# Performance work log

Hardware: AMD Instinct MI355X
Metric: run time of the kernel (lower is better)

## Reference

```python
import jax, jax.numpy as jnp
import numpy as np

B, T, D = 2, 2048, 1024
E, H, K = 8, 2048, 2  # n_experts, expert_dim, n_active_experts


def setup_inputs() -> dict:
    key = jax.random.key(0)
    ks = jax.random.split(key, 5)
    s = 0.02
    return {
        "x": jax.random.normal(ks[0], (B, T, D), dtype=jnp.float32),
        "gate_w": jax.random.normal(ks[1], (E, D), dtype=jnp.float32) * s,
        "w1": jax.random.normal(ks[2], (E, H, D), dtype=jnp.float32) * s,
        "w2": jax.random.normal(ks[3], (E, D, H), dtype=jnp.float32) * s,
        "w3": jax.random.normal(ks[4], (E, H, D), dtype=jnp.float32) * s,
    }


def reference(x, gate_w, w1, w2, w3):
    Bb, Tt, Dd = x.shape
    xf = x.reshape(-1, Dd)                       # [N, D]
    logits = xf @ gate_w.T                       # [N, E]
    probs = jax.nn.softmax(logits, axis=-1)
    vals, idx = jax.lax.top_k(probs, K)          # [N, K]
    w = vals / (vals.sum(-1, keepdims=True) + 1e-8)
    onehot = jax.nn.one_hot(idx, E, dtype=xf.dtype)  # [N, K, E]
    comb = jnp.einsum('nk,nke->ne', w, onehot)   # per-token per-expert combine weight
    # Dense expert eval (same math as masked loop): SwiGLU per expert
    h = jnp.einsum('nd,ehd->neh', xf, w1)        # [N, E, H]
    g = jnp.einsum('nd,ehd->neh', xf, w3)
    eo = jnp.einsum('neh,edh->ned', jax.nn.silu(h) * g, w2)  # [N, E, D]
    out = jnp.einsum('ned,ne->nd', eo, comb)
    return out.reshape(Bb, Tt, Dd)
```

## Files before the change

kernel.cpp:

```cpp
#include <hip/hip_runtime.h>
#include <stdint.h>

#define N_TOK 4096
#define DIM   1024
#define NEXP  8
#define HDIM  2048
#define NSLOT 8192
#define PADSLOT 10240
#define MAXT1 40
#define MAXT2 80

typedef __attribute__((ext_vector_type(8))) short  short8;
typedef __attribute__((ext_vector_type(4))) float  f32x4;

__device__ inline unsigned short f2bf(float f) {
  union { float f; uint32_t u; } v; v.f = f;
  uint32_t u = v.u;
  u += 0x7fffu + ((u >> 16) & 1u);
  return (unsigned short)(u >> 16);
}

__device__ inline void gload_lds16(const void* g, void* l) {
  __builtin_amdgcn_global_load_lds(
      (const __attribute__((address_space(1))) uint32_t*)g,
      (__attribute__((address_space(3))) uint32_t*)l, 16, 0, 0);
}

__global__ __launch_bounds__(256) void cvt_all_kernel(const float* __restrict__ x,
                                                      const float* __restrict__ w1,
                                                      const float* __restrict__ w2,
                                                      const float* __restrict__ w3,
                                                      unsigned short* __restrict__ xb,
                                                      unsigned short* __restrict__ w1b,
                                                      unsigned short* __restrict__ w2b,
                                                      unsigned short* __restrict__ w3b) {
  const int NX = N_TOK * DIM / 4;
  const int NW = NEXP * HDIM * DIM / 4;
  int i = blockIdx.x * blockDim.x + threadIdx.x;
  int stride = gridDim.x * blockDim.x;
  int total = NX + 3 * NW;
  for (; i < total; i += stride) {
    const float* s; unsigned short* d; int j;
    if (i < NX)               { s = x;  d = xb;  j = i; }
    else if (i < NX + NW)     { s = w1; d = w1b; j = i - NX; }
    else if (i < NX + 2 * NW) { s = w2; d = w2b; j = i - NX - NW; }
    else                      { s = w3; d = w3b; j = i - NX - 2 * NW; }
    float4 f = reinterpret_cast<const float4*>(s)[j];
    ushort4 o;
    o.x = f2bf(f.x); o.y = f2bf(f.y); o.z = f2bf(f.z); o.w = f2bf(f.w);
    reinterpret_cast<ushort4*>(d)[j] = o;
  }
}

__global__ __launch_bounds__(256) void gate_kernel(const float* __restrict__ x,
                                                   const float* __restrict__ gw,
                                                   int* __restrict__ tok_e,
                                                   float* __restrict__ tok_w) {
  __shared__ float gws[NEXP * DIM];
  int tid = threadIdx.x;
  for (int i = tid; i < NEXP * DIM; i += 256) gws[i] = gw[i];
  __syncthreads();
  int lane = tid & 63;
  int token = blockIdx.x * 4 + (tid >> 6);
  const float* xr = x + (size_t)token * DIM;
  float acc[NEXP];
#pragma unroll
  for (int e = 0; e < NEXP; ++e) acc[e] = 0.f;
  for (int i = 0; i < DIM / 64; ++i) {
    float xv = xr[i * 64 + lane];
#pragma unroll
    for (int e = 0; e < NEXP; ++e) acc[e] += xv * gws[e * DIM + i * 64 + lane];
  }
#pragma unroll
  for (int off = 32; off > 0; off >>= 1) {
#pragma unroll
    for (int e = 0; e < NEXP; ++e) acc[e] += __shfl_xor(acc[e], off);
  }
  if (lane == 0) {
    float m = acc[0];
#pragma unroll
    for (int e = 1; e < NEXP; ++e) m = fmaxf(m, acc[e]);
    float ex[NEXP], Z = 0.f;
#pragma unroll
    for (int e = 0; e < NEXP; ++e) { ex[e] = expf(acc[e] - m); Z += ex[e]; }
    int b0 = 0; float v0 = ex[0];
#pragma unroll
    for (int e = 1; e < NEXP; ++e) if (ex[e] > v0) { v0 = ex[e]; b0 = e; }
    int b1 = -1; float v1 = -1.f;
#pragma unroll
    for (int e = 0; e < NEXP; ++e) if (e != b0 && ex[e] > v1) { v1 = ex[e]; b1 = e; }
    float p0 = v0 / Z, p1 = v1 / Z;
    float s = p0 + p1 + 1e-8f;
    tok_e[token * 2 + 0] = b0; tok_e[token * 2 + 1] = b1;
    tok_w[token * 2 + 0] = p0 / s; tok_w[token * 2 + 1] = p1 / s;
  }
}

__global__ __launch_bounds__(1024) void route_kernel(const int* __restrict__ tok_e,
                                                     const float* __restrict__ tok_w,
                                                     int* __restrict__ slot_tok,
                                                     float* __restrict__ slot_w,
                                                     int* __restrict__ tile1_e,
                                                     int* __restrict__ tile1_rb,
                                                     int* __restrict__ tile2_e,
                                                     int* __restrict__ tile2_rb,
                                                     int* __restrict__ ntile_g) {
  __shared__ int cnt[NEXP], cur[NEXP];
  __shared__ int total_sh;
  int tid = threadIdx.x;
  if (tid < NEXP) cnt[tid] = 0;
  __syncthreads();
  for (int n = tid; n < N_TOK; n += 1024) {
    atomicAdd(&cnt[tok_e[2 * n]], 1);
    atomicAdd(&cnt[tok_e[2 * n + 1]], 1);
  }
  __syncthreads();
  if (tid == 0) {
    int o = 0, n1 = 0, n2 = 0;
    for (int e = 0; e < NEXP; ++e) {
      cur[e] = o;
      int padded = (cnt[e] + 255) & ~255;
      for (int rb = o; rb < o + padded; rb += 256) { tile1_e[n1] = e; tile1_rb[n1] = rb; ++n1; }
      for (int rb = o; rb < o + padded; rb += 128) { tile2_e[n2] = e; tile2_rb[n2] = rb; ++n2; }
      o += padded;
    }
    ntile_g[0] = n1; ntile_g[1] = n2;
    total_sh = o;
  }
  __syncthreads();
  int total = total_sh;
  for (int s = tid; s < total; s += 1024) { slot_tok[s] = 0; slot_w[s] = 0.f; }
  __syncthreads();
  for (int n = tid; n < N_TOK; n += 1024) {
#pragma unroll
    for (int k = 0; k < 2; ++k) {
      int e = tok_e[2 * n + k];
      int p = atomicAdd(&cur[e], 1);
      slot_tok[p] = n;
      slot_w[p] = tok_w[2 * n + k];
    }
  }
}

__global__ __launch_bounds__(512, 2) void gemm1_kernel(const unsigned short* __restrict__ xb,
                                                       const unsigned short* __restrict__ w1b,
                                                       const unsigned short* __restrict__ w3b,
                                                       const int* __restrict__ slot_tok,
                                                       const int* __restrict__ tile1_e,
                                                       const int* __restrict__ tile1_rb,
                                                       const int* __restrict__ ntile_g,
                                                       unsigned short* __restrict__ hidden) {
  int tile = blockIdx.x >> 4;
  int ct   = blockIdx.x & 15;
  if (tile >= ntile_g[0]) return;
  int e = tile1_e[tile];
  int rowBase = tile1_rb[tile];

  __shared__ alignas(16) unsigned short As[2][256 * 64];
  __shared__ alignas(16) unsigned short B1s[2][128 * 64];
  __shared__ alignas(16) unsigned short B3s[2][128 * 64];
  __shared__ int toks[256];

  int tid = threadIdx.x;
  if (tid < 256) toks[tid] = slot_tok[rowBase + tid];
  __syncthreads();

  int wave = tid >> 6, lane = tid & 63;
  int wr = (wave >> 1) * 64;
  int wc = (wave & 1) * 64;
  int sub = lane >> 3;
  int swcol = (((lane & 7) ^ sub) << 3);

  const size_t wbase = (size_t)e * HDIM * DIM;
  const unsigned short* aptr[4];
  const unsigned short* b1ptr[2];
  const unsigned short* b3ptr[2];
#pragma unroll
  for (int i = 0; i < 4; ++i) {
    int r = (wave + i * 8) * 8 + sub;
    aptr[i] = xb + (size_t)toks[r] * DIM + swcol;
  }
#pragma unroll
  for (int i = 0; i < 2; ++i) {
    int r = (wave + i * 8) * 8 + sub;
    b1ptr[i] = w1b + wbase + (size_t)(ct * 128 + r) * DIM + swcol;
    b3ptr[i] = w3b + wbase + (size_t)(ct * 128 + r) * DIM + swcol;
  }

  f32x4 hacc[4][4], gacc[4][4];
#pragma unroll
  for (int m = 0; m < 4; ++m)
#pragma unroll
    for (int n = 0; n < 4; ++n) {
      hacc[m][n] = (f32x4){0.f, 0.f, 0.f, 0.f};
      gacc[m][n] = (f32x4){0.f, 0.f, 0.f, 0.f};
    }

  gload_lds16(aptr[0], &As[0][(wave + 0) * 512]);
  gload_lds16(aptr[1], &As[0][(wave + 8) * 512]);
  gload_lds16(aptr[2], &As[0][(wave + 16) * 512]);
  gload_lds16(aptr[3], &As[0][(wave + 24) * 512]);
  gload_lds16(b1ptr[0], &B1s[0][wave * 512]);
  gload_lds16(b1ptr[1], &B1s[0][(wave + 8) * 512]);
  gload_lds16(b3ptr[0], &B3s[0][wave * 512]);
  gload_lds16(b3ptr[1], &B3s[0][(wave + 8) * 512]);

  const int NKT = DIM / 64;
  int key = (lane & 7) << 3;
  int l15 = lane & 15;
  int pc0 = ((lane >> 4) * 8) ^ key;
  int pc1 = (32 + (lane >> 4) * 8) ^ key;

  for (int kt = 0; kt < NKT; ++kt) {
    int c = kt & 1;
    int nk = (kt + 1) * 64;
    bool pre = (kt + 1 < NKT);

    __builtin_amdgcn_sched_barrier(0);
    __builtin_amdgcn_s_barrier();
    __builtin_amdgcn_sched_barrier(0);
    if (pre) {
      gload_lds16(aptr[0] + nk, &As[c ^ 1][(wave + 0) * 512]);
      gload_lds16(aptr[1] + nk, &As[c ^ 1][(wave + 8) * 512]);
      asm volatile("s_waitcnt vmcnt(4)" ::: "memory");
    } else {
      asm volatile("s_waitcnt vmcnt(2)" ::: "memory");
    }
    __builtin_amdgcn_sched_barrier(0);
    __builtin_amdgcn_s_barrier();
    __builtin_amdgcn_sched_barrier(0);

    short8 a0[4], a1[4], bv[4];
#pragma unroll
    for (int m = 0; m < 4; ++m)
      a0[m] = *(const short8*)&As[c][(wr + m * 16 + l15) * 64 + pc0];
#pragma unroll
    for (int n = 0; n < 4; ++n)
      bv[n] = *(const short8*)&B1s[c][(wc + n * 16 + l15) * 64 + pc0];
    if (pre) {
      gload_lds16(aptr[2] + nk, &As[c ^ 1][(wave + 16) * 512]);
      gload_lds16(aptr[3] + nk, &As[c ^ 1][(wave + 24) * 512]);
    }
    __builtin_amdgcn_s_setprio(1);
#pragma unroll
    for (int m = 0; m < 4; ++m)
#pragma unroll
      for (int n = 0; n < 4; ++n)
        hacc[m][n] = __builtin_amdgcn_mfma_f32_16x16x32_bf16(a0[m], bv[n], hacc[m][n], 0, 0, 0);
    __builtin_amdgcn_s_setprio(0);

#pragma unroll
    for (int m = 0; m < 4; ++m)
      a1[m] = *(const short8*)&As[c][(wr + m * 16 + l15) * 64 + pc1];
#pragma unroll
    for (int n = 0; n < 4; ++n)
      bv[n] = *(const short8*)&B1s[c][(wc + n * 16 + l15) * 64 + pc1];
    if (pre) {
      gload_lds16(b1ptr[0] + nk, &B1s[c ^ 1][wave * 512]);
      gload_lds16(b1ptr[1] + nk, &B1s[c ^ 1][(wave + 8) * 512]);
    }
    __builtin_amdgcn_s_setprio(1);
#pragma unroll
    for (int m = 0; m < 4; ++m)
#pragma unroll
      for (int n = 0; n < 4; ++n)
        hacc[m][n] = __builtin_amdgcn_mfma_f32_16x16x32_bf16(a1[m], bv[n], hacc[m][n], 0, 0, 0);
    __builtin_amdgcn_s_setprio(0);

    if (pre) asm volatile("s_waitcnt vmcnt(6)" ::: "memory");
    else     asm volatile("s_waitcnt vmcnt(0)" ::: "memory");
    __builtin_amdgcn_sched_barrier(0);
    __builtin_amdgcn_s_barrier();
    __builtin_amdgcn_sched_barrier(0);

#pragma unroll
    for (int n = 0; n < 4; ++n)
      bv[n] = *(const short8*)&B3s[c][(wc + n * 16 + l15) * 64 + pc0];
    if (pre) {
      gload_lds16(b3ptr[0] + nk, &B3s[c ^ 1][wave * 512]);
      gload_lds16(b3ptr[1] + nk, &B3s[c ^ 1][(wave + 8) * 512]);
    }
    __builtin_amdgcn_s_setprio(1);
#pragma unroll
    for (int m = 0; m < 4; ++m)
#pragma unroll
      for (int n = 0; n < 4; ++n)
        gacc[m][n] = __builtin_amdgcn_mfma_f32_16x16x32_bf16(a0[m], bv[n], gacc[m][n], 0, 0, 0);
    __builtin_amdgcn_s_setprio(0);

#pragma unroll
    for (int n = 0; n < 4; ++n)
      bv[n] = *(const short8*)&B3s[c][(wc + n * 16 + l15) * 64 + pc1];
    __builtin_amdgcn_s_setprio(1);
#pragma unroll
    for (int m = 0; m < 4; ++m)
#pragma unroll
      for (int n = 0; n < 4; ++n)
        gacc[m][n] = __builtin_amdgcn_mfma_f32_16x16x32_bf16(a1[m], bv[n], gacc[m][n], 0, 0, 0);
    __builtin_amdgcn_s_setprio(0);
  }

  int cbase = ct * 128 + wc;
#pragma unroll
  for (int m = 0; m < 4; ++m) {
#pragma unroll
    for (int q = 0; q < 4; ++q) {
      int r = wr + m * 16 + ((lane >> 4) * 4 + q);
      size_t rowoff = (size_t)(rowBase + r) * HDIM + cbase;
#pragma unroll
      for (int n = 0; n < 4; ++n) {
        float h = hacc[m][n][q], g = gacc[m][n][q];
        float val = (h / (1.f + expf(-h))) * g;
        hidden[rowoff + n * 16 + (lane & 15)] = f2bf(val);
      }
    }
  }
}

__global__ __launch_bounds__(256, 2) void gemm2_kernel(const unsigned short* __restrict__ hidden,
                                                       const unsigned short* __restrict__ w2b,
                                                       const int* __restrict__ slot_tok,
                                                       const float* __restrict__ slot_w,
                                                       const int* __restrict__ tile2_e,
                                                       const int* __restrict__ tile2_rb,
                                                       const int* __restrict__ ntile_g,
                                                       float* __restrict__ out) {
  int tile = blockIdx.x >> 3;
  int ct   = blockIdx.x & 7;
  if (tile >= ntile_g[1]) return;
  int e = tile2_e[tile];
  int rowBase = tile2_rb[tile];

  __shared__ alignas(16) unsigned short As[2][128 * 64];
  __shared__ alignas(16) unsigned short Bs[2][128 * 64];
  __shared__ int   toks[128];
  __shared__ float wgt[128];

  int tid = threadIdx.x;
  if (tid < 128) {
    toks[tid] = slot_tok[rowBase + tid];
    wgt[tid]  = slot_w[rowBase + tid];
  }
  __syncthreads();

  int wave = tid >> 6, lane = tid & 63;
  int wr = (wave >> 1) * 64, wc = (wave & 1) * 64;
  int sub = lane >> 3;
  int swcol = (((lane & 7) ^ sub) << 3);

  const size_t w2base = (size_t)e * DIM * HDIM;
  const unsigned short* aptr[4];
  const unsigned short* bptr[4];
#pragma unroll
  for (int i = 0; i < 4; ++i) {
    int r = (wave + i * 4) * 8 + sub;
    aptr[i] = hidden + (size_t)(rowBase + r) * HDIM + swcol;
    bptr[i] = w2b + w2base + (size_t)(ct * 128 + r) * HDIM + swcol;
  }

  f32x4 acc[4][4];
#pragma unroll
  for (int m = 0; m < 4; ++m)
#pragma unroll
    for (int n = 0; n < 4; ++n) acc[m][n] = (f32x4){0.f, 0.f, 0.f, 0.f};

#pragma unroll
  for (int i = 0; i < 4; ++i)
    gload_lds16(aptr[i], &As[0][(wave + i * 4) * 512]);
#pragma unroll
  for (int i = 0; i < 4; ++i)
    gload_lds16(bptr[i], &Bs[0][(wave + i * 4) * 512]);

  const int NKT = HDIM / 64;
  int key = (lane & 7) << 3;
  int l15 = lane & 15;
  int pc0 = ((lane >> 4) * 8) ^ key;
  int pc1 = (32 + (lane >> 4) * 8) ^ key;

  for (int kt = 0; kt < NKT; ++kt) {
    int c = kt & 1;
    int nk = (kt + 1) * 64;
    bool pre = (kt + 1 < NKT);

    __builtin_amdgcn_sched_barrier(0);
    __builtin_amdgcn_s_barrier();
    __builtin_amdgcn_sched_barrier(0);
    if (pre) {
#pragma unroll
      for (int i = 0; i < 4; ++i)
        gload_lds16(aptr[i] + nk, &As[c ^ 1][(wave + i * 4) * 512]);
      asm volatile("s_waitcnt vmcnt(4)" ::: "memory");
    } else {
      asm volatile("s_waitcnt vmcnt(0)" ::: "memory");
    }
    __builtin_amdgcn_sched_barrier(0);
    __builtin_amdgcn_s_barrier();
    __builtin_amdgcn_sched_barrier(0);

    short8 a[4], b[4];
#pragma unroll
    for (int m = 0; m < 4; ++m)
      a[m] = *(const short8*)&As[c][(wr + m * 16 + l15) * 64 + pc0];
#pragma unroll
    for (int n = 0; n < 4; ++n)
      b[n] = *(const short8*)&Bs[c][(wc + n * 16 + l15) * 64 + pc0];
    if (pre) {
#pragma unroll
      for (int i = 0; i < 4; ++i)
        gload_lds16(bptr[i] + nk, &Bs[c ^ 1][(wave + i * 4) * 512]);
    }
    __builtin_amdgcn_s_setprio(1);
#pragma unroll
    for (int m = 0; m < 4; ++m)
#pragma unroll
      for (int n = 0; n < 4; ++n)
        acc[m][n] = __builtin_amdgcn_mfma_f32_16x16x32_bf16(a[m], b[n], acc[m][n], 0, 0, 0);
    __builtin_amdgcn_s_setprio(0);

#pragma unroll
    for (int m = 0; m < 4; ++m)
      a[m] = *(const short8*)&As[c][(wr + m * 16 + l15) * 64 + pc1];
#pragma unroll
    for (int n = 0; n < 4; ++n)
      b[n] = *(const short8*)&Bs[c][(wc + n * 16 + l15) * 64 + pc1];
    __builtin_amdgcn_s_setprio(1);
#pragma unroll
    for (int m = 0; m < 4; ++m)
#pragma unroll
      for (int n = 0; n < 4; ++n)
        acc[m][n] = __builtin_amdgcn_mfma_f32_16x16x32_bf16(a[m], b[n], acc[m][n], 0, 0, 0);
    __builtin_amdgcn_s_setprio(0);
  }

  int cbase = ct * 128 + wc;
#pragma unroll
  for (int m = 0; m < 4; ++m) {
#pragma unroll
    for (int q = 0; q < 4; ++q) {
      int r = wr + m * 16 + ((lane >> 4) * 4 + q);
      float w = wgt[r];
      float* orow = out + (size_t)toks[r] * DIM + cbase;
#pragma unroll
      for (int n = 0; n < 4; ++n)
        unsafeAtomicAdd(&orow[n * 16 + (lane & 15)], acc[m][n][q] * w);
    }
  }
}

extern "C" void kernel_launch(void* const* d_in, const int* in_sizes, int n_in,
                              void* d_out, int out_size, void* d_ws, size_t ws_size,
                              hipStream_t stream) {
  const float* x  = (const float*)d_in[0];
  const float* gw = (const float*)d_in[1];
  const float* w1 = (const float*)d_in[2];
  const float* w2 = (const float*)d_in[3];
  const float* w3 = (const float*)d_in[4];
  float* out = (float*)d_out;

  uint8_t* ws = (uint8_t*)d_ws;
  size_t off = 0;
  auto alloc = [&](size_t bytes) -> void* {
    void* p = ws + off; off += (bytes + 255) & ~255ull; return p;
  };
  unsigned short* xb     = (unsigned short*)alloc((size_t)N_TOK * DIM * 2);
  unsigned short* w1b    = (unsigned short*)alloc((size_t)NEXP * HDIM * DIM * 2);
  unsigned short* w3b    = (unsigned short*)alloc((size_t)NEXP * HDIM * DIM * 2);
  unsigned short* w2b    = (unsigned short*)alloc((size_t)NEXP * DIM * HDIM * 2);
  unsigned short* hidden = (unsigned short*)alloc((size_t)PADSLOT * HDIM * 2);
  int*   tok_e    = (int*)alloc(N_TOK * 2 * 4);
  float* tok_w    = (float*)alloc(N_TOK * 2 * 4);
  int*   slot_tok = (int*)alloc(PADSLOT * 4);
  float* slot_w   = (float*)alloc(PADSLOT * 4);
  int*   tile1_e  = (int*)alloc(MAXT1 * 4);
  int*   tile1_rb = (int*)alloc(MAXT1 * 4);
  int*   tile2_e  = (int*)alloc(MAXT2 * 4);
  int*   tile2_rb = (int*)alloc(MAXT2 * 4);
  int*   ntile_g  = (int*)alloc(2 * 4);

  hipMemsetAsync(d_out, 0, (size_t)out_size * sizeof(float), stream);

  cvt_all_kernel<<<2048, 256, 0, stream>>>(x, w1, w2, w3, xb, w1b, w2b, w3b);

  gate_kernel<<<N_TOK / 4, 256, 0, stream>>>(x, gw, tok_e, tok_w);
  route_kernel<<<1, 1024, 0, stream>>>(tok_e, tok_w, slot_tok, slot_w,
                                       tile1_e, tile1_rb, tile2_e, tile2_rb, ntile_g);
  gemm1_kernel<<<MAXT1 * 16, 512, 0, stream>>>(
      xb, w1b, w3b, slot_tok, tile1_e, tile1_rb, ntile_g, hidden);
  gemm2_kernel<<<MAXT2 * 8, 256, 0, stream>>>(
      hidden, w2b, slot_tok, slot_w, tile2_e, tile2_rb, ntile_g, out);
}
```

Measured before the change: 520.5 us.

## Switch expert GEMMs to 4-stage K=32 pipeline and 8-wave gemm2 tiles

```diff
diff --git a/kernel.cpp b/kernel.cpp
--- a/kernel.cpp
+++ b/kernel.cpp
@@ -142,7 +142,7 @@
   }
 }
 
-__global__ __launch_bounds__(512, 2) void gemm1_kernel(const unsigned short* __restrict__ xb,
+__global__ __launch_bounds__(512, 1) void gemm1_kernel(const unsigned short* __restrict__ xb,
                                                        const unsigned short* __restrict__ w1b,
                                                        const unsigned short* __restrict__ w3b,
                                                        const int* __restrict__ slot_tok,
@@ -156,9 +156,9 @@
   int e = tile1_e[tile];
   int rowBase = tile1_rb[tile];
 
-  __shared__ alignas(16) unsigned short As[2][256 * 64];
-  __shared__ alignas(16) unsigned short B1s[2][128 * 64];
-  __shared__ alignas(16) unsigned short B3s[2][128 * 64];
+  __shared__ alignas(16) unsigned short As[4][256 * 32];
+  __shared__ alignas(16) unsigned short B1s[4][128 * 32];
+  __shared__ alignas(16) unsigned short B3s[4][128 * 32];
   __shared__ int toks[256];
 
   int tid = threadIdx.x;
@@ -168,23 +168,23 @@
   int wave = tid >> 6, lane = tid & 63;
   int wr = (wave >> 1) * 64;
   int wc = (wave & 1) * 64;
-  int sub = lane >> 3;
-  int swcol = (((lane & 7) ^ sub) << 3);
+  int r4  = lane >> 2;
+  int cph = lane & 3;
 
   const size_t wbase = (size_t)e * HDIM * DIM;
-  const unsigned short* aptr[4];
-  const unsigned short* b1ptr[2];
-  const unsigned short* b3ptr[2];
-#pragma unroll
-  for (int i = 0; i < 4; ++i) {
-    int r = (wave + i * 8) * 8 + sub;
-    aptr[i] = xb + (size_t)toks[r] * DIM + swcol;
-  }
+  const unsigned short* aptr[2];
+  const unsigned short* b1p;
+  const unsigned short* b3p;
 #pragma unroll
   for (int i = 0; i < 2; ++i) {
-    int r = (wave + i * 8) * 8 + sub;
-    b1ptr[i] = w1b + wbase + (size_t)(ct * 128 + r) * DIM + swcol;
-    b3ptr[i] = w3b + wbase + (size_t)(ct * 128 + r) * DIM + swcol;
+    int r = i * 128 + wave * 16 + r4;
+    aptr[i] = xb + (size_t)toks[r] * DIM + ((cph ^ (r & 3)) << 3);
+  }
+  {
+    int r = wave * 16 + r4;
+    int col = (cph ^ (r & 3)) << 3;
+    b1p = w1b + wbase + (size_t)(ct * 128 + r) * DIM + col;
+    b3p = w3b + wbase + (size_t)(ct * 128 + r) * DIM + col;
   }
 
   f32x4 hacc[4][4], gacc[4][4];
@@ -196,107 +196,58 @@
       gacc[m][n] = (f32x4){0.f, 0.f, 0.f, 0.f};
     }
 
-  gload_lds16(aptr[0], &As[0][(wave + 0) * 512]);
-  gload_lds16(aptr[1], &As[0][(wave + 8) * 512]);
-  gload_lds16(aptr[2], &As[0][(wave + 16) * 512]);
-  gload_lds16(aptr[3], &As[0][(wave + 24) * 512]);
-  gload_lds16(b1ptr[0], &B1s[0][wave * 512]);
-  gload_lds16(b1ptr[1], &B1s[0][(wave + 8) * 512]);
-  gload_lds16(b3ptr[0], &B3s[0][wave * 512]);
-  gload_lds16(b3ptr[1], &B3s[0][(wave + 8) * 512]);
-
-  const int NKT = DIM / 64;
-  int key = (lane & 7) << 3;
+  auto stage = [&](int buf, int kt) {
+    int k0 = kt * 32;
+    gload_lds16(aptr[0] + k0, &As[buf][wave * 512]);
+    gload_lds16(aptr[1] + k0, &As[buf][4096 + wave * 512]);
+    gload_lds16(b1p + k0, &B1s[buf][wave * 512]);
+    gload_lds16(b3p + k0, &B3s[buf][wave * 512]);
+  };
+
+  stage(0, 0); stage(1, 1); stage(2, 2);
+
+  const int NKT = DIM / 32;
   int l15 = lane & 15;
-  int pc0 = ((lane >> 4) * 8) ^ key;
-  int pc1 = (32 + (lane >> 4) * 8) ^ key;
+  int pcoff = (((lane >> 4) ^ (l15 & 3)) << 3);
 
   for (int kt = 0; kt < NKT; ++kt) {
-    int c = kt & 1;
-    int nk = (kt + 1) * 64;
-    bool pre = (kt + 1 < NKT);
+    int c = kt & 3;
+    int rem = NKT - 1 - kt;
 
     __builtin_amdgcn_sched_barrier(0);
     __builtin_amdgcn_s_barrier();
     __builtin_amdgcn_sched_barrier(0);
-    if (pre) {
-      gload_lds16(aptr[0] + nk, &As[c ^ 1][(wave + 0) * 512]);
-      gload_lds16(aptr[1] + nk, &As[c ^ 1][(wave + 8) * 512]);
+    if (rem >= 3) {
+      stage((kt + 3) & 3, kt + 3);
+      asm volatile("s_waitcnt vmcnt(12)" ::: "memory");
+    } else if (rem == 2) {
+      asm volatile("s_waitcnt vmcnt(8)" ::: "memory");
+    } else if (rem == 1) {
       asm volatile("s_waitcnt vmcnt(4)" ::: "memory");
     } else {
-      asm volatile("s_waitcnt vmcnt(2)" ::: "memory");
+      asm volatile("s_waitcnt vmcnt(0)" ::: "memory");
     }
     __builtin_amdgcn_sched_barrier(0);
     __builtin_amdgcn_s_barrier();
     __builtin_amdgcn_sched_barrier(0);
 
-    short8 a0[4], a1[4], bv[4];
+    short8 a[4], b1v[4], b3v[4];
 #pragma unroll
     for (int m = 0; m < 4; ++m)
-      a0[m] = *(const short8*)&As[c][(wr + m * 16 + l15) * 64 + pc0];
-#pragma unroll
-    for (int n = 0; n < 4; ++n)
-      bv[n] = *(const short8*)&B1s[c][(wc + n * 16 + l15) * 64 + pc0];
-    if (pre) {
-      gload_lds16(aptr[2] + nk, &As[c ^ 1][(wave + 16) * 512]);
-      gload_lds16(aptr[3] + nk, &As[c ^ 1][(wave + 24) * 512]);
+      a[m] = *(const short8*)&As[c][(wr + m * 16 + l15) * 32 + pcoff];
+#pragma unroll
+    for (int n = 0; n < 4; ++n) {
+      b1v[n] = *(const short8*)&B1s[c][(wc + n * 16 + l15) * 32 + pcoff];
+      b3v[n] = *(const short8*)&B3s[c][(wc + n * 16 + l15) * 32 + pcoff];
     }
     __builtin_amdgcn_s_setprio(1);
 #pragma unroll
     for (int m = 0; m < 4; ++m)
 #pragma unroll
-      for (int n = 0; n < 4; ++n)
-        hacc[m][n] = __builtin_amdgcn_mfma_f32_16x16x32_bf16(a0[m], bv[n], hacc[m][n], 0, 0, 0);
-    __builtin_amdgcn_s_setprio(0);
-
-#pragma unroll
-    for (int m = 0; m < 4; ++m)
-      a1[m] = *(const short8*)&As[c][(wr + m * 16 + l15) * 64 + pc1];
-#pragma unroll
-    for (int n = 0; n < 4; ++n)
-      bv[n] = *(const short8*)&B1s[c][(wc + n * 16 + l15) * 64 + pc1];
-    if (pre) {
-      gload_lds16(b1ptr[0] + nk, &B1s[c ^ 1][wave * 512]);
-      gload_lds16(b1ptr[1] + nk, &B1s[c ^ 1][(wave + 8) * 512]);
-    }
-    __builtin_amdgcn_s_setprio(1);
-#pragma unroll
-    for (int m = 0; m < 4; ++m)
-#pragma unroll
-      for (int n = 0; n < 4; ++n)
-        hacc[m][n] = __builtin_amdgcn_mfma_f32_16x16x32_bf16(a1[m], bv[n], hacc[m][n], 0, 0, 0);
-    __builtin_amdgcn_s_setprio(0);
-
-    if (pre) asm volatile("s_waitcnt vmcnt(6)" ::: "memory");
-    else     asm volatile("s_waitcnt vmcnt(0)" ::: "memory");
-    __builtin_amdgcn_sched_barrier(0);
-    __builtin_amdgcn_s_barrier();
-    __builtin_amdgcn_sched_barrier(0);
-
-#pragma unroll
-    for (int n = 0; n < 4; ++n)
-      bv[n] = *(const short8*)&B3s[c][(wc + n * 16 + l15) * 64 + pc0];
-    if (pre) {
-      gload_lds16(b3ptr[0] + nk, &B3s[c ^ 1][wave * 512]);
-      gload_lds16(b3ptr[1] + nk, &B3s[c ^ 1][(wave + 8) * 512]);
-    }
-    __builtin_amdgcn_s_setprio(1);
-#pragma unroll
-    for (int m = 0; m < 4; ++m)
-#pragma unroll
-      for (int n = 0; n < 4; ++n)
-        gacc[m][n] = __builtin_amdgcn_mfma_f32_16x16x32_bf16(a0[m], bv[n], gacc[m][n], 0, 0, 0);
-    __builtin_amdgcn_s_setprio(0);
-
-#pragma unroll
-    for (int n = 0; n < 4; ++n)
-      bv[n] = *(const short8*)&B3s[c][(wc + n * 16 + l15) * 64 + pc1];
-    __builtin_amdgcn_s_setprio(1);
-#pragma unroll
-    for (int m = 0; m < 4; ++m)
-#pragma unroll
-      for (int n = 0; n < 4; ++n)
-        gacc[m][n] = __builtin_amdgcn_mfma_f32_16x16x32_bf16(a1[m], bv[n], gacc[m][n], 0, 0, 0);
+      for (int n = 0; n < 4; ++n) {
+        hacc[m][n] = __builtin_amdgcn_mfma_f32_16x16x32_bf16(a[m], b1v[n], hacc[m][n], 0, 0, 0);
+        gacc[m][n] = __builtin_amdgcn_mfma_f32_16x16x32_bf16(a[m], b3v[n], gacc[m][n], 0, 0, 0);
+      }
     __builtin_amdgcn_s_setprio(0);
   }
 
@@ -317,7 +268,7 @@
   }
 }
 
-__global__ __launch_bounds__(256, 2) void gemm2_kernel(const unsigned short* __restrict__ hidden,
+__global__ __launch_bounds__(512, 2) void gemm2_kernel(const unsigned short* __restrict__ hidden,
                                                        const unsigned short* __restrict__ w2b,
                                                        const int* __restrict__ slot_tok,
                                                        const float* __restrict__ slot_w,
@@ -331,8 +282,8 @@
   int e = tile2_e[tile];
   int rowBase = tile2_rb[tile];
 
-  __shared__ alignas(16) unsigned short As[2][128 * 64];
-  __shared__ alignas(16) unsigned short Bs[2][128 * 64];
+  __shared__ alignas(16) unsigned short As[4][128 * 32];
+  __shared__ alignas(16) unsigned short Bs[4][128 * 32];
   __shared__ int   toks[128];
   __shared__ float wgt[128];
 
@@ -344,52 +295,53 @@
   __syncthreads();
 
   int wave = tid >> 6, lane = tid & 63;
-  int wr = (wave >> 1) * 64, wc = (wave & 1) * 64;
-  int sub = lane >> 3;
-  int swcol = (((lane & 7) ^ sub) << 3);
+  int wr = (wave >> 2) * 64;
+  int wc = (wave & 3) * 32;
+  int r4  = lane >> 2;
+  int cph = lane & 3;
 
   const size_t w2base = (size_t)e * DIM * HDIM;
-  const unsigned short* aptr[4];
-  const unsigned short* bptr[4];
-#pragma unroll
-  for (int i = 0; i < 4; ++i) {
-    int r = (wave + i * 4) * 8 + sub;
-    aptr[i] = hidden + (size_t)(rowBase + r) * HDIM + swcol;
-    bptr[i] = w2b + w2base + (size_t)(ct * 128 + r) * HDIM + swcol;
-  }
-
-  f32x4 acc[4][4];
+  const unsigned short* aptr;
+  const unsigned short* bptr;
+  {
+    int r = wave * 16 + r4;
+    int col = (cph ^ (r & 3)) << 3;
+    aptr = hidden + (size_t)(rowBase + r) * HDIM + col;
+    bptr = w2b + w2base + (size_t)(ct * 128 + r) * HDIM + col;
+  }
+
+  f32x4 acc[4][2];
 #pragma unroll
   for (int m = 0; m < 4; ++m)
 #pragma unroll
-    for (int n = 0; n < 4; ++n) acc[m][n] = (f32x4){0.f, 0.f, 0.f, 0.f};
-
-#pragma unroll
-  for (int i = 0; i < 4; ++i)
-    gload_lds16(aptr[i], &As[0][(wave + i * 4) * 512]);
-#pragma unroll
-  for (int i = 0; i < 4; ++i)
-    gload_lds16(bptr[i], &Bs[0][(wave + i * 4) * 512]);
-
-  const int NKT = HDIM / 64;
-  int key = (lane & 7) << 3;
+    for (int n = 0; n < 2; ++n) acc[m][n] = (f32x4){0.f, 0.f, 0.f, 0.f};
+
+  auto stage = [&](int buf, int kt) {
+    int k0 = kt * 32;
+    gload_lds16(aptr + k0, &As[buf][wave * 512]);
+    gload_lds16(bptr + k0, &Bs[buf][wave * 512]);
+  };
+
+  stage(0, 0); stage(1, 1); stage(2, 2);
+
+  const int NKT = HDIM / 32;
   int l15 = lane & 15;
-  int pc0 = ((lane >> 4) * 8) ^ key;
-  int pc1 = (32 + (lane >> 4) * 8) ^ key;
+  int pcoff = (((lane >> 4) ^ (l15 & 3)) << 3);
 
   for (int kt = 0; kt < NKT; ++kt) {
-    int c = kt & 1;
-    int nk = (kt + 1) * 64;
-    bool pre = (kt + 1 < NKT);
+    int c = kt & 3;
+    int rem = NKT - 1 - kt;
 
     __builtin_amdgcn_sched_barrier(0);
     __builtin_amdgcn_s_barrier();
     __builtin_amdgcn_sched_barrier(0);
-    if (pre) {
-#pragma unroll
-      for (int i = 0; i < 4; ++i)
-        gload_lds16(aptr[i] + nk, &As[c ^ 1][(wave + i * 4) * 512]);
+    if (rem >= 3) {
+      stage((kt + 3) & 3, kt + 3);
+      asm volatile("s_waitcnt vmcnt(6)" ::: "memory");
+    } else if (rem == 2) {
       asm volatile("s_waitcnt vmcnt(4)" ::: "memory");
+    } else if (rem == 1) {
+      asm volatile("s_waitcnt vmcnt(2)" ::: "memory");
     } else {
       asm volatile("s_waitcnt vmcnt(0)" ::: "memory");
     }
@@ -397,37 +349,18 @@
     __builtin_amdgcn_s_barrier();
     __builtin_amdgcn_sched_barrier(0);
 
-    short8 a[4], b[4];
+    short8 a[4], b[2];
 #pragma unroll
     for (int m = 0; m < 4; ++m)
-      a[m] = *(const short8*)&As[c][(wr + m * 16 + l15) * 64 + pc0];
-#pragma unroll
-    for (int n = 0; n < 4; ++n)
-      b[n] = *(const short8*)&Bs[c][(wc + n * 16 + l15) * 64 + pc0];
-    if (pre) {
-#pragma unroll
-      for (int i = 0; i < 4; ++i)
-        gload_lds16(bptr[i] + nk, &Bs[c ^ 1][(wave + i * 4) * 512]);
-    }
+      a[m] = *(const short8*)&As[c][(wr + m * 16 + l15) * 32 + pcoff];
+#pragma unroll
+    for (int n = 0; n < 2; ++n)
+      b[n] = *(const short8*)&Bs[c][(wc + n * 16 + l15) * 32 + pcoff];
     __builtin_amdgcn_s_setprio(1);
 #pragma unroll
     for (int m = 0; m < 4; ++m)
 #pragma unroll
-      for (int n = 0; n < 4; ++n)
-        acc[m][n] = __builtin_amdgcn_mfma_f32_16x16x32_bf16(a[m], b[n], acc[m][n], 0, 0, 0);
-    __builtin_amdgcn_s_setprio(0);
-
-#pragma unroll
-    for (int m = 0; m < 4; ++m)
-      a[m] = *(const short8*)&As[c][(wr + m * 16 + l15) * 64 + pc1];
-#pragma unroll
-    for (int n = 0; n < 4; ++n)
-      b[n] = *(const short8*)&Bs[c][(wc + n * 16 + l15) * 64 + pc1];
-    __builtin_amdgcn_s_setprio(1);
-#pragma unroll
-    for (int m = 0; m < 4; ++m)
-#pragma unroll
-      for (int n = 0; n < 4; ++n)
+      for (int n = 0; n < 2; ++n)
         acc[m][n] = __builtin_amdgcn_mfma_f32_16x16x32_bf16(a[m], b[n], acc[m][n], 0, 0, 0);
     __builtin_amdgcn_s_setprio(0);
   }
@@ -441,7 +374,7 @@
       float w = wgt[r];
       float* orow = out + (size_t)toks[r] * DIM + cbase;
 #pragma unroll
-      for (int n = 0; n < 4; ++n)
+      for (int n = 0; n < 2; ++n)
         unsafeAtomicAdd(&orow[n * 16 + (lane & 15)], acc[m][n][q] * w);
     }
   }
@@ -486,6 +419,6 @@
                                        tile1_e, tile1_rb, tile2_e, tile2_rb, ntile_g);
   gemm1_kernel<<<MAXT1 * 16, 512, 0, stream>>>(
       xb, w1b, w3b, slot_tok, tile1_e, tile1_rb, ntile_g, hidden);
-  gemm2_kernel<<<MAXT2 * 8, 256, 0, stream>>>(
+  gemm2_kernel<<<MAXT2 * 8, 512, 0, stream>>>(
       hidden, w2b, slot_tok, slot_w, tile2_e, tile2_rb, ntile_g, out);
 }
```

Measured after the change: 541.6 us. +4.1%, slower.
